# Performance work log

Measured on AMD Instinct MI355X. Metric: run time of the kernel, lower is better.

Reference implementation:

```python
import jax, jax.numpy as jnp
import numpy as np

N, C, NE = 65536, 128, 10
INV_SQ2 = float(1.0 / np.sqrt(2.0))   # path weight sqrt(ir_out.dim / n_paths) * w3j, 0e outputs
INV_SQ6 = float(1.0 / np.sqrt(6.0))   # sqrt(1/2) * 1/sqrt(3) for the 1o.1o->0e dot path


def _fcn(x, weights):
    # e3nn FullyConnectedNet: no biases, fan-in normalized, silu between layers
    h = x
    for i, W in enumerate(weights):
        h = (h @ W) * float(1.0 / np.sqrt(W.shape[0]))
        if i < len(weights) - 1:
            h = jax.nn.silu(h)
    return h


def setup_inputs() -> dict:
    key = jax.random.key(0)
    ks = jax.random.split(key, 24)
    elem = jax.random.randint(ks[0], (N,), 0, NE)
    return {
        'node_feats_s': jax.random.normal(ks[1], (N, C), jnp.float32),
        'node_feats_v': jax.random.normal(ks[2], (N, C, 3), jnp.float32),
        'sc': jax.random.normal(ks[3], (N, 4 * C), jnp.float32),
        'node_attrs': jax.nn.one_hot(elem, NE, dtype=jnp.float32),
        'magmom_node_inv_feats': jax.random.normal(ks[4], (N, 16), jnp.float32),
        'magmom_node_attrs': jax.random.normal(ks[5], (N, 4), jnp.float32),
        'magmom_lenghts': jax.random.uniform(ks[6], (N, 1), jnp.float32),
        'Ws': jax.random.normal(ks[7], (NE, 5, C), jnp.float32),
        'Wv': jax.random.normal(ks[8], (NE, 4, C), jnp.float32),
        'Wc1': jax.random.normal(ks[9], (16, 64), jnp.float32),
        'Wc2': jax.random.normal(ks[10], (64, 64), jnp.float32),
        'Wc3': jax.random.normal(ks[11], (64, 64), jnp.float32),
        'Wc4': jax.random.normal(ks[12], (64, 4 * C), jnp.float32),
        'Wb1': jax.random.normal(ks[13], (16, 64), jnp.float32),
        'Wb2': jax.random.normal(ks[14], (64, 64), jnp.float32),
        'Wb3': jax.random.normal(ks[15], (64, 64), jnp.float32),
        'Wb4': jax.random.normal(ks[16], (64, C), jnp.float32),
        'exp_scaling': jnp.full((1,), 5.0, jnp.float32),
        'Wl0': jax.random.normal(ks[17], (2 * C, C), jnp.float32),
        'Wl1': jax.random.normal(ks[18], (2 * C, C), jnp.float32),
        'Wo0': jax.random.normal(ks[19], (C, C), jnp.float32),
        'Wo1': jax.random.normal(ks[20], (C, C), jnp.float32),
    }


def reference(node_feats_s, node_feats_v, sc, node_attrs, magmom_node_inv_feats,
              magmom_node_attrs, magmom_lenghts, Ws, Wv, Wc1, Wc2, Wc3, Wc4,
              Wb1, Wb2, Wb3, Wb4, exp_scaling, Wl0, Wl1, Wo0, Wo1):
    s, v = node_feats_s, node_feats_v                     # [N,C], [N,C,3]
    # --- SymmetricContraction (correlation 3, l<=1): per-element weighted symmetric CG basis ---
    ws = jnp.einsum('ne,epc->npc', node_attrs, Ws)        # [N,5,C] element-selected weights
    wv = jnp.einsum('ne,epc->npc', node_attrs, Wv)        # [N,4,C]
    vv = jnp.sum(v * v, axis=-1)                          # [N,C] invariant |v|^2
    out_s = (ws[:, 0] * s + ws[:, 1] * (s * s) + ws[:, 2] * vv
             + ws[:, 3] * (s * s * s) + ws[:, 4] * (s * vv))
    gate = wv[:, 0] + wv[:, 1] * s + wv[:, 2] * (s * s) + wv[:, 3] * vv
    out_v = gate[..., None] * v                           # [N,C,3] all 1o basis terms are multiples of v
    # --- conv_tp weights from invariant magmom feats ---
    tp_w = _fcn(magmom_node_inv_feats, [Wc1, Wc2, Wc3, Wc4])   # [N,4C]
    w0, w1, w2, w3 = (tp_w[:, 0:C], tp_w[:, C:2 * C], tp_w[:, 2 * C:3 * C], tp_w[:, 3 * C:4 * C])
    y0 = magmom_node_attrs[:, 0:1]                        # 1x0e
    y1 = magmom_node_attrs[:, 1:4]                        # 1x1o
    # --- path-sparse TensorProduct (uvu, per-sample weights), 4 instructions ---
    m0 = INV_SQ2 * w0 * out_s * y0                                     # 0e x 0e -> 0e
    m1 = INV_SQ6 * w1 * jnp.einsum('nci,ni->nc', out_v, y1)           # 1o x 1o -> 0e
    m2 = INV_SQ2 * w2[..., None] * out_s[..., None] * y1[:, None, :]  # 0e x 1o -> 1o
    m3 = INV_SQ2 * w3[..., None] * out_v * y0[:, :, None]             # 1o x 0e -> 1o
    # --- one-body magmom basis added to the scalar channels ---
    ob = _fcn(magmom_node_inv_feats, [Wb1, Wb2, Wb3, Wb4])            # [N,C]
    m0 = m0 + (1.0 - jnp.exp(-exp_scaling * magmom_lenghts)) * ob
    # --- equivariant Linear(irreps_mid -> target) + Linear(target -> target) + sc ---
    scal = jnp.concatenate([m0, m1], axis=1)              # [N,2C] 0e block
    vecs = jnp.concatenate([m2, m3], axis=1)              # [N,2C,3] 1o block
    inv_2c = float(1.0 / np.sqrt(2 * C))
    inv_c = float(1.0 / np.sqrt(C))
    out0 = (scal @ Wl0) * inv_2c
    out1 = jnp.einsum('nci,co->noi', vecs, Wl1) * inv_2c
    o0 = (out_s @ Wo0) * inv_c
    o1 = jnp.einsum('nci,co->noi', out_v, Wo1) * inv_c
    msg0 = out0 + o0 + sc[:, :C]
    msg1 = (out1 + o1).reshape(-1, 3 * C) + sc[:, C:]
    return jnp.concatenate([msg0, msg1], axis=1)          # [N, 4C] = target_irreps.dim
```

## Files before the change

### kernel.cpp

```cpp
#include <hip/hip_runtime.h>

#define NNODES 65536
#define CC 128
#define NEL 10
#define BN 32
#define NT 512

#define INV_SQ2f 0.70710678118654752440f
#define INV_SQ6f 0.40824829046386301637f
#define INV_2Cf  0.0625f
#define INV_Cf   0.08838834764831845f
#define S16f 0.25f
#define S64f 0.125f

#define WS_FRAGS 312
#define WS_BYTES (WS_FRAGS * 1024)

typedef __attribute__((ext_vector_type(8))) short s16x8;
typedef __attribute__((ext_vector_type(4))) float f32x4;
#define MFMA16(a, b, c) __builtin_amdgcn_mfma_f32_16x16x32_bf16((a), (b), (c), 0, 0, 0)

union U8 { unsigned short u[8]; s16x8 s; };

__device__ __forceinline__ unsigned short bf16rne(float x) {
    unsigned int u = __float_as_uint(x);
    return (unsigned short)((u + 0x7FFFu + ((u >> 16) & 1u)) >> 16);
}
__device__ __forceinline__ float bf2f(unsigned short h) {
    return __uint_as_float(((unsigned int)h) << 16);
}
__device__ __forceinline__ unsigned int packbf(float a, float b) {
    return (unsigned int)bf16rne(a) | (((unsigned int)bf16rne(b)) << 16);
}
__device__ __forceinline__ float siluf(float x) {
    return x * (1.0f / (1.0f + __expf(-x)));
}

extern "C" __global__ void prep_frags(
    const float* __restrict__ WC1, const float* __restrict__ WC2,
    const float* __restrict__ WC3, const float* __restrict__ WB1,
    const float* __restrict__ WB2, const float* __restrict__ WB3,
    const float* __restrict__ WC4, const float* __restrict__ WB4,
    const float* __restrict__ WL0, const float* __restrict__ WO0,
    const float* __restrict__ WL1, const float* __restrict__ WO1,
    unsigned short* __restrict__ wsb)
{
    const int b = blockIdx.x;
    const int l = threadIdx.x;
    const float* W; int K, N, nKS, base; float sc;
    if      (b <  4) { W = WC1; K = 16;  N = 64;  nKS = 1; base = 0;   sc = S16f; }
    else if (b < 12) { W = WC2; K = 64;  N = 64;  nKS = 2; base = 4;   sc = S64f; }
    else if (b < 20) { W = WC3; K = 64;  N = 64;  nKS = 2; base = 12;  sc = S64f; }
    else if (b < 24) { W = WB1; K = 16;  N = 64;  nKS = 1; base = 20;  sc = S16f; }
    else if (b < 32) { W = WB2; K = 64;  N = 64;  nKS = 2; base = 24;  sc = S64f; }
    else if (b < 40) { W = WB3; K = 64;  N = 64;  nKS = 2; base = 32;  sc = S64f; }
    else if (b < 104){ W = WC4; K = 64;  N = 512; nKS = 2; base = 40;  sc = S64f; }
    else if (b < 120){ W = WB4; K = 64;  N = 128; nKS = 2; base = 104; sc = S64f; }
    else if (b < 184){ W = WL0; K = 256; N = 128; nKS = 8; base = 120; sc = INV_2Cf; }
    else if (b < 216){ W = WO0; K = 128; N = 128; nKS = 4; base = 184; sc = INV_Cf; }
    else if (b < 280){ W = WL1; K = 256; N = 128; nKS = 8; base = 216; sc = INV_2Cf; }
    else             { W = WO1; K = 128; N = 128; nKS = 4; base = 280; sc = INV_Cf; }
    const int f  = b - base;
    const int nt = f / nKS, ks = f % nKS;
    const int n  = nt * 16 + (l & 15);
    const int k0 = ks * 32 + (l >> 4) * 8;
    U8 v;
    #pragma unroll
    for (int j = 0; j < 8; ++j) {
        const int k = k0 + j;
        const float x = (k < K) ? W[(size_t)k * N + n] * sc : 0.0f;
        v.u[j] = bf16rne(x);
    }
    *(s16x8*)(wsb + (size_t)b * 512 + l * 8) = v.s;
}

__device__ __forceinline__ s16x8 ldB(const unsigned short* __restrict__ wsb, int fragidx, int lane) {
    return *(const s16x8*)(wsb + ((size_t)fragidx << 9) + lane * 8);
}
__device__ __forceinline__ s16x8 ldA136(const unsigned short* X, int row, int ks, int gq) {
    return *(const s16x8*)(X + row * 136 + ks * 32 + gq * 8);
}
__device__ __forceinline__ s16x8 ldA72(const unsigned short* X, int row, int ks, int gq) {
    return *(const s16x8*)(X + row * 72 + ks * 32 + gq * 8);
}

extern "C" __global__ void __launch_bounds__(NT)
epb_mfma(const float* __restrict__ Sin, const float* __restrict__ Vin,
         const float* __restrict__ SCp, const float* __restrict__ ATT,
         const float* __restrict__ INVF, const float* __restrict__ MNA,
         const float* __restrict__ MLEN, const float* __restrict__ WSp,
         const float* __restrict__ WVp, const float* __restrict__ ESC,
         const unsigned short* __restrict__ wsb, float* __restrict__ OUT)
{
    extern __shared__ char smem[];
    unsigned short* B1 = (unsigned short*)smem;
    unsigned short* B2 = B1 + 4352;
    unsigned short* B3 = B2 + 4352;
    unsigned short* B4 = B3 + 4352;
    unsigned short* B5 = B4 + 4352;
    unsigned short* B6 = B5 + 4352;
    float* y0f  = (float*)(smem + 6 * 8704);
    float* y1f  = y0f + 32;
    float* etf  = y1f + 96;

    const int tid  = threadIdx.x;
    const int n0   = blockIdx.x * BN;
    const int w    = tid >> 6;
    const int lane = tid & 63;
    const int cl   = lane & 15;
    const int gq   = lane >> 4;
    const int T    = w;
    const int mch  = w >> 2;
    const int mt   = w & 3;
    const f32x4 Z4 = {0.f, 0.f, 0.f, 0.f};

    U8 invu[2];
    #pragma unroll
    for (int rg = 0; rg < 2; ++rg) {
        if (gq < 2) {
            const float* ip = INVF + (size_t)(n0 + rg * 16 + cl) * 16 + gq * 8;
            #pragma unroll
            for (int j = 0; j < 8; ++j) invu[rg].u[j] = bf16rne(ip[j]);
        } else {
            #pragma unroll
            for (int j = 0; j < 8; ++j) invu[rg].u[j] = 0;
        }
    }

    if (tid < BN) {
        const int gn = n0 + tid;
        y0f[tid] = MNA[gn * 4 + 0];
        y1f[tid * 3 + 0] = MNA[gn * 4 + 1];
        y1f[tid * 3 + 1] = MNA[gn * 4 + 2];
        y1f[tid * 3 + 2] = MNA[gn * 4 + 3];
        etf[tid] = 1.0f - __expf(-ESC[0] * MLEN[gn]);
    }

    {
        unsigned short* Hd = mch ? B2 : B1;
        const int fi = (mch ? 20 : 0) + mt;
        #pragma unroll
        for (int rg = 0; rg < 2; ++rg) {
            const f32x4 c = MFMA16(invu[rg].s, ldB(wsb, fi, lane), Z4);
            #pragma unroll
            for (int r = 0; r < 4; ++r) {
                const int rw = rg * 16 + gq * 4 + r;
                Hd[rw * 72 + mt * 16 + cl] = bf16rne(siluf(c[r]));
            }
        }
    }
    __syncthreads();

    {
        const unsigned short* Hs = mch ? B2 : B1;
        unsigned short* Hd = mch ? B4 : B3;
        const int base = mch ? 24 : 4;
        f32x4 c[2] = {Z4, Z4};
        #pragma unroll
        for (int ks = 0; ks < 2; ++ks) {
            const s16x8 f = ldB(wsb, base + mt * 2 + ks, lane);
            #pragma unroll
            for (int rg = 0; rg < 2; ++rg)
                c[rg] = MFMA16(ldA72(Hs, rg * 16 + cl, ks, gq), f, c[rg]);
        }
        #pragma unroll
        for (int rg = 0; rg < 2; ++rg)
            #pragma unroll
            for (int r = 0; r < 4; ++r) {
                const int rw = rg * 16 + gq * 4 + r;
                Hd[rw * 72 + mt * 16 + cl] = bf16rne(siluf(c[rg][r]));
            }
    }
    __syncthreads();

    {
        const unsigned short* Hs = mch ? B4 : B3;
        unsigned short* Hd = mch ? B6 : B5;
        const int base = mch ? 32 : 12;
        f32x4 c[2] = {Z4, Z4};
        #pragma unroll
        for (int ks = 0; ks < 2; ++ks) {
            const s16x8 f = ldB(wsb, base + mt * 2 + ks, lane);
            #pragma unroll
            for (int rg = 0; rg < 2; ++rg)
                c[rg] = MFMA16(ldA72(Hs, rg * 16 + cl, ks, gq), f, c[rg]);
        }
        #pragma unroll
        for (int rg = 0; rg < 2; ++rg)
            #pragma unroll
            for (int r = 0; r < 4; ++r) {
                const int rw = rg * 16 + gq * 4 + r;
                Hd[rw * 72 + mt * 16 + cl] = bf16rne(siluf(c[rg][r]));
            }
    }
    __syncthreads();

    s16x8 h3c[2][2], h3b[2][2];
    #pragma unroll
    for (int rg = 0; rg < 2; ++rg)
        #pragma unroll
        for (int ks = 0; ks < 2; ++ks) {
            h3c[rg][ks] = ldA72(B5, rg * 16 + cl, ks, gq);
            h3b[rg][ks] = ldA72(B6, rg * 16 + cl, ks, gq);
        }
    f32x4 obacc[2];
    {
        const s16x8 f0 = ldB(wsb, 104 + T * 2 + 0, lane);
        const s16x8 f1 = ldB(wsb, 104 + T * 2 + 1, lane);
        #pragma unroll
        for (int rg = 0; rg < 2; ++rg)
            obacc[rg] = MFMA16(h3b[rg][1], f1, MFMA16(h3b[rg][0], f0, Z4));
    }

    unsigned int vpack[3][4];
    {
        const int row = tid >> 4;
        const int c0  = (tid & 15) << 3;
        const size_t gn = (size_t)(n0 + row);
        const float4 mna = *(const float4*)(MNA + gn * 4);
        const float y10 = mna.y, y11 = mna.z, y12 = mna.w;
        int e = 0;
        #pragma unroll
        for (int k = 0; k < NEL; ++k)
            if (ATT[gn * NEL + k] > 0.5f) e = k;
        const float* sp  = Sin + gn * CC + c0;
        const float* vp  = Vin + (gn * CC + c0) * 3;
        const float* wsp = WSp + ((size_t)e * 5) * CC + c0;
        const float* wvp = WVp + ((size_t)e * 4) * CC + c0;
        unsigned int* B1d = (unsigned int*)B1;
        unsigned int* B2d = (unsigned int*)B2;
        unsigned int* B3d = (unsigned int*)B3;
        const int dbase = row * 68 + (c0 >> 1);
        #pragma unroll
        for (int jp = 0; jp < 4; ++jp) {
            const int c = 2 * jp;
            const float2 s2 = *(const float2*)(sp + c);
            const float2 va = *(const float2*)(vp + 3 * c);
            const float2 vb = *(const float2*)(vp + 3 * c + 2);
            const float2 vc = *(const float2*)(vp + 3 * c + 4);
            vpack[0][jp] = packbf(va.x, vb.y);
            vpack[1][jp] = packbf(va.y, vc.x);
            vpack[2][jp] = packbf(vb.x, vc.y);
            const float vv0 = va.x * va.x + va.y * va.y + vb.x * vb.x;
            const float vv1 = vb.y * vb.y + vc.x * vc.x + vc.y * vc.y;
            const float vy0 = va.x * y10 + va.y * y11 + vb.x * y12;
            const float vy1 = vb.y * y10 + vc.x * y11 + vc.y * y12;
            const float2 p0 = *(const float2*)(wsp + 0 * CC + c);
            const float2 p1 = *(const float2*)(wsp + 1 * CC + c);
            const float2 p2 = *(const float2*)(wsp + 2 * CC + c);
            const float2 p3 = *(const float2*)(wsp + 3 * CC + c);
            const float2 p4 = *(const float2*)(wsp + 4 * CC + c);
            const float2 q0 = *(const float2*)(wvp + 0 * CC + c);
            const float2 q1 = *(const float2*)(wvp + 1 * CC + c);
            const float2 q2 = *(const float2*)(wvp + 2 * CC + c);
            const float2 q3 = *(const float2*)(wvp + 3 * CC + c);
            const float s0 = s2.x, s1 = s2.y;
            const float ss0 = s0 * s0, ss1 = s1 * s1;
            const float os0 = p0.x * s0 + p1.x * ss0 + p2.x * vv0 + p3.x * (ss0 * s0) + p4.x * (s0 * vv0);
            const float os1 = p0.y * s1 + p1.y * ss1 + p2.y * vv1 + p3.y * (ss1 * s1) + p4.y * (s1 * vv1);
            const float gt0 = q0.x + q1.x * s0 + q2.x * ss0 + q3.x * vv0;
            const float gt1 = q0.y + q1.y * s1 + q2.y * ss1 + q3.y * vv1;
            B1d[dbase + jp] = packbf(os0, os1);
            B2d[dbase + jp] = packbf(gt0, gt1);
            B3d[dbase + jp] = packbf(vy0, vy1);
        }
    }
    __syncthreads();

#define WCHUNK(q, wc)                                                          \
    {                                                                          \
        const s16x8 f0 = ldB(wsb, 40 + ((q) * 8 + T) * 2 + 0, lane);           \
        const s16x8 f1 = ldB(wsb, 40 + ((q) * 8 + T) * 2 + 1, lane);           \
        _Pragma("unroll")                                                      \
        for (int rg = 0; rg < 2; ++rg)                                         \
            wc[rg] = MFMA16(h3c[rg][1], f1, MFMA16(h3c[rg][0], f0, Z4));       \
    }
    {
        f32x4 wc[2];
        WCHUNK(0, wc)
        #pragma unroll
        for (int rg = 0; rg < 2; ++rg)
            #pragma unroll
            for (int r = 0; r < 4; ++r) {
                const int rw = rg * 16 + gq * 4 + r;
                const int col = T * 16 + cl;
                const float os = bf2f(B1[rw * 136 + col]);
                B4[rw * 136 + col] = bf16rne(INV_SQ2f * wc[rg][r] * os * y0f[rw]
                                             + etf[rw] * obacc[rg][r]);
            }
        WCHUNK(1, wc)
        #pragma unroll
        for (int rg = 0; rg < 2; ++rg)
            #pragma unroll
            for (int r = 0; r < 4; ++r) {
                const int rw = rg * 16 + gq * 4 + r;
                const int col = T * 16 + cl;
                const float gt = bf2f(B2[rw * 136 + col]);
                const float vy = bf2f(B3[rw * 136 + col]);
                B3[rw * 136 + col] = bf16rne(INV_SQ6f * wc[rg][r] * gt * vy);
            }
        WCHUNK(2, wc)
        #pragma unroll
        for (int rg = 0; rg < 2; ++rg)
            #pragma unroll
            for (int r = 0; r < 4; ++r) {
                const int rw = rg * 16 + gq * 4 + r;
                const int col = T * 16 + cl;
                B6[rw * 136 + col] = bf16rne(INV_SQ2f * wc[rg][r] * bf2f(B1[rw * 136 + col]));
            }
        WCHUNK(3, wc)
        #pragma unroll
        for (int rg = 0; rg < 2; ++rg)
            #pragma unroll
            for (int r = 0; r < 4; ++r) {
                const int rw = rg * 16 + gq * 4 + r;
                const int col = T * 16 + cl;
                const float gt = bf2f(B2[rw * 136 + col]);
                B5[rw * 136 + col] = bf16rne(INV_SQ2f * wc[rg][r] * gt * y0f[rw]);
            }
    }
#undef WCHUNK
    __syncthreads();

    f32x4 tacc[2] = {Z4, Z4};
    {
        f32x4 acc[2] = {Z4, Z4};
        #pragma unroll
        for (int ks = 0; ks < 12; ++ks) {
            const unsigned short* Xa = (ks < 4) ? B4 : (ks < 8) ? B3 : B1;
            const int fi = (ks < 8) ? (120 + T * 8 + ks) : (184 + T * 4 + (ks - 8));
            const s16x8 bfrag = ldB(wsb, fi, lane);
            #pragma unroll
            for (int rg = 0; rg < 2; ++rg)
                acc[rg] = MFMA16(ldA136(Xa, rg * 16 + cl, ks & 3, gq), bfrag, acc[rg]);
        }
        #pragma unroll
        for (int ks = 0; ks < 4; ++ks) {
            const s16x8 bfrag = ldB(wsb, 216 + T * 8 + ks, lane);
            #pragma unroll
            for (int rg = 0; rg < 2; ++rg)
                tacc[rg] = MFMA16(ldA136(B6, rg * 16 + cl, ks, gq), bfrag, tacc[rg]);
        }
        #pragma unroll
        for (int rg = 0; rg < 2; ++rg)
            #pragma unroll
            for (int r = 0; r < 4; ++r) {
                const int rw = rg * 16 + gq * 4 + r;
                const size_t o = (size_t)(n0 + rw) * 512 + T * 16 + cl;
                OUT[o] = acc[rg][r] + SCp[o];
            }
    }
    __syncthreads();

    f32x4 acc3[3][2];

#define STAGE_I(i, DSTB, DSTG)                                                  \
    {                                                                           \
        const int dbase = (tid >> 4) * 68 + (tid & 15) * 4;                     \
        const unsigned int* bD = (const unsigned int*)B5;                       \
        const unsigned int* gD = (const unsigned int*)B2;                       \
        unsigned int* o1 = (unsigned int*)(DSTB);                               \
        unsigned int* o3 = (unsigned int*)(DSTG);                               \
        _Pragma("unroll")                                                       \
        for (int jp = 0; jp < 4; ++jp) {                                        \
            const unsigned int bd = bD[dbase + jp];                             \
            const unsigned int gd = gD[dbase + jp];                             \
            const float v0 = bf2f((unsigned short)(vpack[i][jp] & 0xffff));     \
            const float v1 = bf2f((unsigned short)(vpack[i][jp] >> 16));        \
            o1[dbase + jp] = packbf(bf2f((unsigned short)(bd & 0xffff)) * v0,   \
                                    bf2f((unsigned short)(bd >> 16)) * v1);     \
            o3[dbase + jp] = packbf(bf2f((unsigned short)(gd & 0xffff)) * v0,   \
                                    bf2f((unsigned short)(gd >> 16)) * v1);     \
        }                                                                       \
    }

#define GEMM_I(i, SRCB, SRCG)                                                   \
    {                                                                           \
        _Pragma("unroll")                                                       \
        for (int rg = 0; rg < 2; ++rg) acc3[i][rg] = Z4;                        \
        _Pragma("unroll")                                                       \
        for (int ks = 0; ks < 4; ++ks) {                                        \
            const s16x8 fb = ldB(wsb, 216 + T * 8 + 4 + ks, lane);              \
            const s16x8 fg = ldB(wsb, 280 + T * 4 + ks, lane);                  \
            _Pragma("unroll")                                                   \
            for (int rg = 0; rg < 2; ++rg) {                                    \
                acc3[i][rg] = MFMA16(ldA136((SRCB), rg * 16 + cl, ks, gq), fb, acc3[i][rg]); \
                acc3[i][rg] = MFMA16(ldA136((SRCG), rg * 16 + cl, ks, gq), fg, acc3[i][rg]); \
            }                                                                   \
        }                                                                       \
    }

    STAGE_I(0, B1, B3)
    __syncthreads();
    GEMM_I(0, B1, B3)
    STAGE_I(1, B4, B6)
    __syncthreads();
    GEMM_I(1, B4, B6)
    STAGE_I(2, B1, B3)
    __syncthreads();
    GEMM_I(2, B1, B3)

    #pragma unroll
    for (int rg = 0; rg < 2; ++rg)
        #pragma unroll
        for (int r = 0; r < 4; ++r) {
            const int rw = rg * 16 + gq * 4 + r;
            const int col = T * 16 + cl;
            const size_t o = (size_t)(n0 + rw) * 512 + 128 + (size_t)col * 3;
            const float tv = tacc[rg][r];
            OUT[o + 0] = acc3[0][rg][r] + tv * y1f[rw * 3 + 0] + SCp[o + 0];
            OUT[o + 1] = acc3[1][rg][r] + tv * y1f[rw * 3 + 1] + SCp[o + 1];
            OUT[o + 2] = acc3[2][rg][r] + tv * y1f[rw * 3 + 2] + SCp[o + 2];
        }
#undef STAGE_I
#undef GEMM_I
}

extern "C" void kernel_launch(void* const* d_in, const int* in_sizes, int n_in,
                              void* d_out, int out_size, void* d_ws, size_t ws_size,
                              hipStream_t stream)
{
    (void)in_sizes; (void)n_in; (void)out_size; (void)ws_size;
    const float* Sin  = (const float*)d_in[0];
    const float* Vin  = (const float*)d_in[1];
    const float* SCp  = (const float*)d_in[2];
    const float* ATT  = (const float*)d_in[3];
    const float* INVF = (const float*)d_in[4];
    const float* MNA  = (const float*)d_in[5];
    const float* MLEN = (const float*)d_in[6];
    const float* WSp  = (const float*)d_in[7];
    const float* WVp  = (const float*)d_in[8];
    const float* WC1  = (const float*)d_in[9];
    const float* WC2  = (const float*)d_in[10];
    const float* WC3  = (const float*)d_in[11];
    const float* WC4  = (const float*)d_in[12];
    const float* WB1  = (const float*)d_in[13];
    const float* WB2  = (const float*)d_in[14];
    const float* WB3  = (const float*)d_in[15];
    const float* WB4  = (const float*)d_in[16];
    const float* ESC  = (const float*)d_in[17];
    const float* WL0  = (const float*)d_in[18];
    const float* WL1  = (const float*)d_in[19];
    const float* WO0  = (const float*)d_in[20];
    const float* WO1  = (const float*)d_in[21];
    float* OUT = (float*)d_out;

    unsigned short* wsb = (unsigned short*)d_ws;
    hipLaunchKernelGGL(prep_frags, dim3(WS_FRAGS), dim3(64), 0, stream,
                       WC1, WC2, WC3, WB1, WB2, WB3, WC4, WB4,
                       WL0, WO0, WL1, WO1, wsb);
    const size_t shbytes = (size_t)(6 * 8704 + 768);
    hipLaunchKernelGGL(epb_mfma, dim3(NNODES / BN), dim3(NT), shbytes, stream,
                       Sin, Vin, SCp, ATT, INVF, MNA, MLEN, WSp, WVp, ESC,
                       wsb, OUT);
}
```

Before: 184.3 us.

## Restructure fused kernel into single-wave blocks of 16 nodes without barriers

Replaces the 512-thread, 32-node block with a single 64-lane wave that handles 16 nodes and loops over all output tiles itself, so every __syncthreads becomes a compiler fence. LDS use drops from six buffers to four smaller ones, which allows more blocks per CU, and the three vector-component GEMMs reuse the same staging buffers one after another. The cost is that each wave now loads every weight fragment for all eight column tiles with no reuse across waves, and it holds many more accumulators and a larger vpack array in registers, which may cut occupancy.

```diff
diff --git a/kernel.cpp b/kernel.cpp
--- a/kernel.cpp
+++ b/kernel.cpp
@@ -3,8 +3,8 @@
 #define NNODES 65536
 #define CC 128
 #define NEL 10
-#define BN 32
-#define NT 512
+#define BN 16
+#define NT 64
 
 #define INV_SQ2f 0.70710678118654752440f
 #define INV_SQ6f 0.40824829046386301637f
@@ -14,7 +14,8 @@
 #define S64f 0.125f
 
 #define WS_FRAGS 312
-#define WS_BYTES (WS_FRAGS * 1024)
+
+#define CFENCE() asm volatile("" ::: "memory")
 
 typedef __attribute__((ext_vector_type(8))) short s16x8;
 typedef __attribute__((ext_vector_type(4))) float f32x4;
@@ -85,7 +86,7 @@
 }
 
 extern "C" __global__ void __launch_bounds__(NT)
-epb_mfma(const float* __restrict__ Sin, const float* __restrict__ Vin,
+epb_wave(const float* __restrict__ Sin, const float* __restrict__ Vin,
          const float* __restrict__ SCp, const float* __restrict__ ATT,
          const float* __restrict__ INVF, const float* __restrict__ MNA,
          const float* __restrict__ MLEN, const float* __restrict__ WSp,
@@ -94,128 +95,103 @@
 {
     extern __shared__ char smem[];
     unsigned short* B1 = (unsigned short*)smem;
-    unsigned short* B2 = B1 + 4352;
-    unsigned short* B3 = B2 + 4352;
-    unsigned short* B4 = B3 + 4352;
-    unsigned short* B5 = B4 + 4352;
-    unsigned short* B6 = B5 + 4352;
-    float* y0f  = (float*)(smem + 6 * 8704);
-    float* y1f  = y0f + 32;
-    float* etf  = y1f + 96;
-
-    const int tid  = threadIdx.x;
-    const int n0   = blockIdx.x * BN;
-    const int w    = tid >> 6;
-    const int lane = tid & 63;
+    unsigned short* B2 = B1 + 2176;
+    unsigned short* B3 = B2 + 2176;
+    unsigned short* B4 = B3 + 2176;
+    float* y0f = (float*)(smem + 4 * 4352);
+    float* y1f = y0f + 16;
+    float* etf = y1f + 48;
+
+    const int lane = threadIdx.x;
     const int cl   = lane & 15;
     const int gq   = lane >> 4;
-    const int T    = w;
-    const int mch  = w >> 2;
-    const int mt   = w & 3;
+    const int n0   = blockIdx.x * BN;
     const f32x4 Z4 = {0.f, 0.f, 0.f, 0.f};
 
-    U8 invu[2];
-    #pragma unroll
-    for (int rg = 0; rg < 2; ++rg) {
-        if (gq < 2) {
-            const float* ip = INVF + (size_t)(n0 + rg * 16 + cl) * 16 + gq * 8;
-            #pragma unroll
-            for (int j = 0; j < 8; ++j) invu[rg].u[j] = bf16rne(ip[j]);
-        } else {
-            #pragma unroll
-            for (int j = 0; j < 8; ++j) invu[rg].u[j] = 0;
-        }
-    }
-
-    if (tid < BN) {
-        const int gn = n0 + tid;
-        y0f[tid] = MNA[gn * 4 + 0];
-        y1f[tid * 3 + 0] = MNA[gn * 4 + 1];
-        y1f[tid * 3 + 1] = MNA[gn * 4 + 2];
-        y1f[tid * 3 + 2] = MNA[gn * 4 + 3];
-        etf[tid] = 1.0f - __expf(-ESC[0] * MLEN[gn]);
-    }
-
-    {
-        unsigned short* Hd = mch ? B2 : B1;
-        const int fi = (mch ? 20 : 0) + mt;
-        #pragma unroll
-        for (int rg = 0; rg < 2; ++rg) {
-            const f32x4 c = MFMA16(invu[rg].s, ldB(wsb, fi, lane), Z4);
-            #pragma unroll
-            for (int r = 0; r < 4; ++r) {
-                const int rw = rg * 16 + gq * 4 + r;
-                Hd[rw * 72 + mt * 16 + cl] = bf16rne(siluf(c[r]));
-            }
-        }
-    }
-    __syncthreads();
-
-    {
-        const unsigned short* Hs = mch ? B2 : B1;
-        unsigned short* Hd = mch ? B4 : B3;
-        const int base = mch ? 24 : 4;
-        f32x4 c[2] = {Z4, Z4};
+    U8 invu;
+    if (gq < 2) {
+        const float* ip = INVF + (size_t)(n0 + cl) * 16 + gq * 8;
+        #pragma unroll
+        for (int j = 0; j < 8; ++j) invu.u[j] = bf16rne(ip[j]);
+    } else {
+        #pragma unroll
+        for (int j = 0; j < 8; ++j) invu.u[j] = 0;
+    }
+
+    if (lane < BN) {
+        const int gn = n0 + lane;
+        y0f[lane] = MNA[gn * 4 + 0];
+        y1f[lane * 3 + 0] = MNA[gn * 4 + 1];
+        y1f[lane * 3 + 1] = MNA[gn * 4 + 2];
+        y1f[lane * 3 + 2] = MNA[gn * 4 + 3];
+        etf[lane] = 1.0f - __expf(-ESC[0] * MLEN[gn]);
+    }
+    CFENCE();
+
+    #pragma unroll
+    for (int mt = 0; mt < 4; ++mt) {
+        const f32x4 c = MFMA16(invu.s, ldB(wsb, 0 + mt, lane), Z4);
+        const f32x4 b = MFMA16(invu.s, ldB(wsb, 20 + mt, lane), Z4);
+        #pragma unroll
+        for (int r = 0; r < 4; ++r) {
+            const int rw = gq * 4 + r;
+            B1[rw * 72 + mt * 16 + cl] = bf16rne(siluf(c[r]));
+            B2[rw * 72 + mt * 16 + cl] = bf16rne(siluf(b[r]));
+        }
+    }
+    CFENCE();
+    #pragma unroll
+    for (int mt = 0; mt < 4; ++mt) {
+        f32x4 c = Z4, b = Z4;
         #pragma unroll
         for (int ks = 0; ks < 2; ++ks) {
-            const s16x8 f = ldB(wsb, base + mt * 2 + ks, lane);
-            #pragma unroll
-            for (int rg = 0; rg < 2; ++rg)
-                c[rg] = MFMA16(ldA72(Hs, rg * 16 + cl, ks, gq), f, c[rg]);
-        }
-        #pragma unroll
-        for (int rg = 0; rg < 2; ++rg)
-            #pragma unroll
-            for (int r = 0; r < 4; ++r) {
-                const int rw = rg * 16 + gq * 4 + r;
-                Hd[rw * 72 + mt * 16 + cl] = bf16rne(siluf(c[rg][r]));
-            }
-    }
-    __syncthreads();
-
-    {
-        const unsigned short* Hs = mch ? B4 : B3;
-        unsigned short* Hd = mch ? B6 : B5;
-        const int base = mch ? 32 : 12;
-        f32x4 c[2] = {Z4, Z4};
+            c = MFMA16(ldA72(B1, cl, ks, gq), ldB(wsb, 4 + mt * 2 + ks, lane), c);
+            b = MFMA16(ldA72(B2, cl, ks, gq), ldB(wsb, 24 + mt * 2 + ks, lane), b);
+        }
+        #pragma unroll
+        for (int r = 0; r < 4; ++r) {
+            const int rw = gq * 4 + r;
+            B3[rw * 72 + mt * 16 + cl] = bf16rne(siluf(c[r]));
+            B4[rw * 72 + mt * 16 + cl] = bf16rne(siluf(b[r]));
+        }
+    }
+    CFENCE();
+    #pragma unroll
+    for (int mt = 0; mt < 4; ++mt) {
+        f32x4 c = Z4, b = Z4;
         #pragma unroll
         for (int ks = 0; ks < 2; ++ks) {
-            const s16x8 f = ldB(wsb, base + mt * 2 + ks, lane);
-            #pragma unroll
-            for (int rg = 0; rg < 2; ++rg)
-                c[rg] = MFMA16(ldA72(Hs, rg * 16 + cl, ks, gq), f, c[rg]);
-        }
-        #pragma unroll
-        for (int rg = 0; rg < 2; ++rg)
-            #pragma unroll
-            for (int r = 0; r < 4; ++r) {
-                const int rw = rg * 16 + gq * 4 + r;
-                Hd[rw * 72 + mt * 16 + cl] = bf16rne(siluf(c[rg][r]));
-            }
-    }
-    __syncthreads();
-
-    s16x8 h3c[2][2], h3b[2][2];
-    #pragma unroll
-    for (int rg = 0; rg < 2; ++rg)
-        #pragma unroll
-        for (int ks = 0; ks < 2; ++ks) {
-            h3c[rg][ks] = ldA72(B5, rg * 16 + cl, ks, gq);
-            h3b[rg][ks] = ldA72(B6, rg * 16 + cl, ks, gq);
-        }
-    f32x4 obacc[2];
-    {
+            c = MFMA16(ldA72(B3, cl, ks, gq), ldB(wsb, 12 + mt * 2 + ks, lane), c);
+            b = MFMA16(ldA72(B4, cl, ks, gq), ldB(wsb, 32 + mt * 2 + ks, lane), b);
+        }
+        #pragma unroll
+        for (int r = 0; r < 4; ++r) {
+            const int rw = gq * 4 + r;
+            B1[rw * 72 + mt * 16 + cl] = bf16rne(siluf(c[r]));
+            B2[rw * 72 + mt * 16 + cl] = bf16rne(siluf(b[r]));
+        }
+    }
+    CFENCE();
+
+    s16x8 h3c[2], h3b[2];
+    #pragma unroll
+    for (int ks = 0; ks < 2; ++ks) {
+        h3c[ks] = ldA72(B1, cl, ks, gq);
+        h3b[ks] = ldA72(B2, cl, ks, gq);
+    }
+    CFENCE();
+    f32x4 obacc[8];
+    #pragma unroll
+    for (int T = 0; T < 8; ++T) {
         const s16x8 f0 = ldB(wsb, 104 + T * 2 + 0, lane);
         const s16x8 f1 = ldB(wsb, 104 + T * 2 + 1, lane);
-        #pragma unroll
-        for (int rg = 0; rg < 2; ++rg)
-            obacc[rg] = MFMA16(h3b[rg][1], f1, MFMA16(h3b[rg][0], f0, Z4));
-    }
-
-    unsigned int vpack[3][4];
+        obacc[T] = MFMA16(h3b[1], f1, MFMA16(h3b[0], f0, Z4));
+    }
+
+    unsigned int vpack[3][16];
     {
-        const int row = tid >> 4;
-        const int c0  = (tid & 15) << 3;
+        const int row = lane >> 2;
+        const int c0  = (lane & 3) << 5;
         const size_t gn = (size_t)(n0 + row);
         const float4 mna = *(const float4*)(MNA + gn * 4);
         const float y10 = mna.y, y11 = mna.z, y12 = mna.w;
@@ -232,7 +208,7 @@
         unsigned int* B3d = (unsigned int*)B3;
         const int dbase = row * 68 + (c0 >> 1);
         #pragma unroll
-        for (int jp = 0; jp < 4; ++jp) {
+        for (int jp = 0; jp < 16; ++jp) {
             const int c = 2 * jp;
             const float2 s2 = *(const float2*)(sp + c);
             const float2 va = *(const float2*)(vp + 3 * c);
@@ -265,155 +241,127 @@
             B3d[dbase + jp] = packbf(vy0, vy1);
         }
     }
-    __syncthreads();
-
-#define WCHUNK(q, wc)                                                          \
+    CFENCE();
+
+#define WCHUNK(q, T, wc)                                                       \
     {                                                                          \
-        const s16x8 f0 = ldB(wsb, 40 + ((q) * 8 + T) * 2 + 0, lane);           \
-        const s16x8 f1 = ldB(wsb, 40 + ((q) * 8 + T) * 2 + 1, lane);           \
-        _Pragma("unroll")                                                      \
-        for (int rg = 0; rg < 2; ++rg)                                         \
-            wc[rg] = MFMA16(h3c[rg][1], f1, MFMA16(h3c[rg][0], f0, Z4));       \
-    }
+        const s16x8 f0 = ldB(wsb, 40 + ((q) * 8 + (T)) * 2 + 0, lane);         \
+        const s16x8 f1 = ldB(wsb, 40 + ((q) * 8 + (T)) * 2 + 1, lane);         \
+        wc = MFMA16(h3c[1], f1, MFMA16(h3c[0], f0, Z4));                       \
+    }
+
+    #pragma unroll
+    for (int T = 0; T < 8; ++T) {
+        f32x4 wc0, wc1;
+        WCHUNK(0, T, wc0)
+        WCHUNK(1, T, wc1)
+        #pragma unroll
+        for (int r = 0; r < 4; ++r) {
+            const int rw = gq * 4 + r;
+            const int col = T * 16 + cl;
+            const float os = bf2f(B1[rw * 136 + col]);
+            B4[rw * 136 + col] = bf16rne(INV_SQ2f * wc0[r] * os * y0f[rw]
+                                         + etf[rw] * obacc[T][r]);
+            const float gt = bf2f(B2[rw * 136 + col]);
+            const float vy = bf2f(B3[rw * 136 + col]);
+            B3[rw * 136 + col] = bf16rne(INV_SQ6f * wc1[r] * gt * vy);
+        }
+    }
+    CFENCE();
+
     {
-        f32x4 wc[2];
-        WCHUNK(0, wc)
-        #pragma unroll
-        for (int rg = 0; rg < 2; ++rg)
+        f32x4 acc[8] = {Z4, Z4, Z4, Z4, Z4, Z4, Z4, Z4};
+        #pragma unroll
+        for (int ks = 0; ks < 12; ++ks) {
+            const unsigned short* Xa = (ks < 4) ? B4 : (ks < 8) ? B3 : B1;
+            const s16x8 a = ldA136(Xa, cl, ks & 3, gq);
+            #pragma unroll
+            for (int T = 0; T < 8; ++T) {
+                const int fi = (ks < 8) ? (120 + T * 8 + ks) : (184 + T * 4 + (ks - 8));
+                acc[T] = MFMA16(a, ldB(wsb, fi, lane), acc[T]);
+            }
+        }
+        #pragma unroll
+        for (int T = 0; T < 8; ++T)
             #pragma unroll
             for (int r = 0; r < 4; ++r) {
-                const int rw = rg * 16 + gq * 4 + r;
-                const int col = T * 16 + cl;
-                const float os = bf2f(B1[rw * 136 + col]);
-                B4[rw * 136 + col] = bf16rne(INV_SQ2f * wc[rg][r] * os * y0f[rw]
-                                             + etf[rw] * obacc[rg][r]);
+                const int rw = gq * 4 + r;
+                const size_t o = (size_t)(n0 + rw) * 512 + T * 16 + cl;
+                OUT[o] = acc[T][r] + SCp[o];
             }
-        WCHUNK(1, wc)
-        #pragma unroll
-        for (int rg = 0; rg < 2; ++rg)
+    }
+    CFENCE();
+
+    #pragma unroll
+    for (int T = 0; T < 8; ++T) {
+        f32x4 wc2, wc3;
+        WCHUNK(2, T, wc2)
+        WCHUNK(3, T, wc3)
+        #pragma unroll
+        for (int r = 0; r < 4; ++r) {
+            const int rw = gq * 4 + r;
+            const int col = T * 16 + cl;
+            B4[rw * 136 + col] = bf16rne(INV_SQ2f * wc2[r] * bf2f(B1[rw * 136 + col]));
+            const float gt = bf2f(B2[rw * 136 + col]);
+            B3[rw * 136 + col] = bf16rne(INV_SQ2f * wc3[r] * gt * y0f[rw]);
+        }
+    }
+#undef WCHUNK
+    CFENCE();
+
+    f32x4 tacc[8] = {Z4, Z4, Z4, Z4, Z4, Z4, Z4, Z4};
+    #pragma unroll
+    for (int ks = 0; ks < 4; ++ks) {
+        const s16x8 a = ldA136(B4, cl, ks, gq);
+        #pragma unroll
+        for (int T = 0; T < 8; ++T)
+            tacc[T] = MFMA16(a, ldB(wsb, 216 + T * 8 + ks, lane), tacc[T]);
+    }
+    CFENCE();
+
+    #pragma unroll
+    for (int i = 0; i < 3; ++i) {
+        {
+            const int dbase = (lane >> 2) * 68 + (lane & 3) * 16;
+            const unsigned int* bD = (const unsigned int*)B3;
+            const unsigned int* gD = (const unsigned int*)B2;
+            unsigned int* o1 = (unsigned int*)B1;
+            unsigned int* o4 = (unsigned int*)B4;
+            #pragma unroll
+            for (int jp = 0; jp < 16; ++jp) {
+                const unsigned int bd = bD[dbase + jp];
+                const unsigned int gd = gD[dbase + jp];
+                const float v0 = bf2f((unsigned short)(vpack[i][jp] & 0xffff));
+                const float v1 = bf2f((unsigned short)(vpack[i][jp] >> 16));
+                o1[dbase + jp] = packbf(bf2f((unsigned short)(bd & 0xffff)) * v0,
+                                        bf2f((unsigned short)(bd >> 16)) * v1);
+                o4[dbase + jp] = packbf(bf2f((unsigned short)(gd & 0xffff)) * v0,
+                                        bf2f((unsigned short)(gd >> 16)) * v1);
+            }
+        }
+        CFENCE();
+        f32x4 a3[8] = {Z4, Z4, Z4, Z4, Z4, Z4, Z4, Z4};
+        #pragma unroll
+        for (int ks = 0; ks < 4; ++ks) {
+            const s16x8 a1 = ldA136(B1, cl, ks, gq);
+            const s16x8 ag = ldA136(B4, cl, ks, gq);
+            #pragma unroll
+            for (int T = 0; T < 8; ++T) {
+                a3[T] = MFMA16(a1, ldB(wsb, 216 + T * 8 + 4 + ks, lane), a3[T]);
+                a3[T] = MFMA16(ag, ldB(wsb, 280 + T * 4 + ks, lane), a3[T]);
+            }
+        }
+        CFENCE();
+        #pragma unroll
+        for (int T = 0; T < 8; ++T)
             #pragma unroll
             for (int r = 0; r < 4; ++r) {
-                const int rw = rg * 16 + gq * 4 + r;
+                const int rw = gq * 4 + r;
                 const int col = T * 16 + cl;
-                const float gt = bf2f(B2[rw * 136 + col]);
-                const float vy = bf2f(B3[rw * 136 + col]);
-                B3[rw * 136 + col] = bf16rne(INV_SQ6f * wc[rg][r] * gt * vy);
+                const size_t o = (size_t)(n0 + rw) * 512 + 128 + (size_t)col * 3 + i;
+                OUT[o] = a3[T][r] + tacc[T][r] * y1f[rw * 3 + i] + SCp[o];
             }
-        WCHUNK(2, wc)
-        #pragma unroll
-        for (int rg = 0; rg < 2; ++rg)
-            #pragma unroll
-            for (int r = 0; r < 4; ++r) {
-                const int rw = rg * 16 + gq * 4 + r;
-                const int col = T * 16 + cl;
-                B6[rw * 136 + col] = bf16rne(INV_SQ2f * wc[rg][r] * bf2f(B1[rw * 136 + col]));
-            }
-        WCHUNK(3, wc)
-        #pragma unroll
-        for (int rg = 0; rg < 2; ++rg)
-            #pragma unroll
-            for (int r = 0; r < 4; ++r) {
-                const int rw = rg * 16 + gq * 4 + r;
-                const int col = T * 16 + cl;
-                const float gt = bf2f(B2[rw * 136 + col]);
-                B5[rw * 136 + col] = bf16rne(INV_SQ2f * wc[rg][r] * gt * y0f[rw]);
-            }
-    }
-#undef WCHUNK
-    __syncthreads();
-
-    f32x4 tacc[2] = {Z4, Z4};
-    {
-        f32x4 acc[2] = {Z4, Z4};
-        #pragma unroll
-        for (int ks = 0; ks < 12; ++ks) {
-            const unsigned short* Xa = (ks < 4) ? B4 : (ks < 8) ? B3 : B1;
-            const int fi = (ks < 8) ? (120 + T * 8 + ks) : (184 + T * 4 + (ks - 8));
-            const s16x8 bfrag = ldB(wsb, fi, lane);
-            #pragma unroll
-            for (int rg = 0; rg < 2; ++rg)
-                acc[rg] = MFMA16(ldA136(Xa, rg * 16 + cl, ks & 3, gq), bfrag, acc[rg]);
-        }
-        #pragma unroll
-        for (int ks = 0; ks < 4; ++ks) {
-            const s16x8 bfrag = ldB(wsb, 216 + T * 8 + ks, lane);
-            #pragma unroll
-            for (int rg = 0; rg < 2; ++rg)
-                tacc[rg] = MFMA16(ldA136(B6, rg * 16 + cl, ks, gq), bfrag, tacc[rg]);
-        }
-        #pragma unroll
-        for (int rg = 0; rg < 2; ++rg)
-            #pragma unroll
-            for (int r = 0; r < 4; ++r) {
-                const int rw = rg * 16 + gq * 4 + r;
-                const size_t o = (size_t)(n0 + rw) * 512 + T * 16 + cl;
-                OUT[o] = acc[rg][r] + SCp[o];
-            }
-    }
-    __syncthreads();
-
-    f32x4 acc3[3][2];
-
-#define STAGE_I(i, DSTB, DSTG)                                                  \
-    {                                                                           \
-        const int dbase = (tid >> 4) * 68 + (tid & 15) * 4;                     \
-        const unsigned int* bD = (const unsigned int*)B5;                       \
-        const unsigned int* gD = (const unsigned int*)B2;                       \
-        unsigned int* o1 = (unsigned int*)(DSTB);                               \
-        unsigned int* o3 = (unsigned int*)(DSTG);                               \
-        _Pragma("unroll")                                                       \
-        for (int jp = 0; jp < 4; ++jp) {                                        \
-            const unsigned int bd = bD[dbase + jp];                             \
-            const unsigned int gd = gD[dbase + jp];                             \
-            const float v0 = bf2f((unsigned short)(vpack[i][jp] & 0xffff));     \
-            const float v1 = bf2f((unsigned short)(vpack[i][jp] >> 16));        \
-            o1[dbase + jp] = packbf(bf2f((unsigned short)(bd & 0xffff)) * v0,   \
-                                    bf2f((unsigned short)(bd >> 16)) * v1);     \
-            o3[dbase + jp] = packbf(bf2f((unsigned short)(gd & 0xffff)) * v0,   \
-                                    bf2f((unsigned short)(gd >> 16)) * v1);     \
-        }                                                                       \
-    }
-
-#define GEMM_I(i, SRCB, SRCG)                                                   \
-    {                                                                           \
-        _Pragma("unroll")                                                       \
-        for (int rg = 0; rg < 2; ++rg) acc3[i][rg] = Z4;                        \
-        _Pragma("unroll")                                                       \
-        for (int ks = 0; ks < 4; ++ks) {                                        \
-            const s16x8 fb = ldB(wsb, 216 + T * 8 + 4 + ks, lane);              \
-            const s16x8 fg = ldB(wsb, 280 + T * 4 + ks, lane);                  \
-            _Pragma("unroll")                                                   \
-            for (int rg = 0; rg < 2; ++rg) {                                    \
-                acc3[i][rg] = MFMA16(ldA136((SRCB), rg * 16 + cl, ks, gq), fb, acc3[i][rg]); \
-                acc3[i][rg] = MFMA16(ldA136((SRCG), rg * 16 + cl, ks, gq), fg, acc3[i][rg]); \
-            }                                                                   \
-        }                                                                       \
-    }
-
-    STAGE_I(0, B1, B3)
-    __syncthreads();
-    GEMM_I(0, B1, B3)
-    STAGE_I(1, B4, B6)
-    __syncthreads();
-    GEMM_I(1, B4, B6)
-    STAGE_I(2, B1, B3)
-    __syncthreads();
-    GEMM_I(2, B1, B3)
-
-    #pragma unroll
-    for (int rg = 0; rg < 2; ++rg)
-        #pragma unroll
-        for (int r = 0; r < 4; ++r) {
-            const int rw = rg * 16 + gq * 4 + r;
-            const int col = T * 16 + cl;
-            const size_t o = (size_t)(n0 + rw) * 512 + 128 + (size_t)col * 3;
-            const float tv = tacc[rg][r];
-            OUT[o + 0] = acc3[0][rg][r] + tv * y1f[rw * 3 + 0] + SCp[o + 0];
-            OUT[o + 1] = acc3[1][rg][r] + tv * y1f[rw * 3 + 1] + SCp[o + 1];
-            OUT[o + 2] = acc3[2][rg][r] + tv * y1f[rw * 3 + 2] + SCp[o + 2];
-        }
-#undef STAGE_I
-#undef GEMM_I
+    }
 }
 
 extern "C" void kernel_launch(void* const* d_in, const int* in_sizes, int n_in,
@@ -449,8 +397,8 @@
     hipLaunchKernelGGL(prep_frags, dim3(WS_FRAGS), dim3(64), 0, stream,
                        WC1, WC2, WC3, WB1, WB2, WB3, WC4, WB4,
                        WL0, WO0, WL1, WO1, wsb);
-    const size_t shbytes = (size_t)(6 * 8704 + 768);
-    hipLaunchKernelGGL(epb_mfma, dim3(NNODES / BN), dim3(NT), shbytes, stream,
+    const size_t shbytes = (size_t)(4 * 4352 + 320);
+    hipLaunchKernelGGL(epb_wave, dim3(NNODES / BN), dim3(NT), shbytes, stream,
                        Sin, Vin, SCp, ATT, INVF, MNA, MLEN, WSp, WVp, ESC,
                        wsb, OUT);
 }
```

After: 371.7 us. 2.02x slower.
